# Performance work log

Hardware: AMD Instinct MI355X
Metric: run time of the kernel (lower is better)

Reference implementation:

```python
import jax, jax.numpy as jnp
import numpy as np

P = 1024   # number of partitions / local models (n_terms)
K = 9      # local neighborhood size (in_dim of each LocalDNN)
W = 10     # LocalDNN width
B = 16384  # batch
F = 1024   # input feature dim (lattice sites)


def setup_inputs() -> dict:
    key = jax.random.key(0)
    ks = jax.random.split(key, 9)
    x = jax.random.normal(ks[0], (B, F), dtype=jnp.float32)
    idx = jax.random.randint(ks[1], (P, K), 0, F)  # parameter_map: per-partition feature indices
    # stacked LocalDNN parameters (one tiny MLP per partition)
    s1 = 1.0 / np.sqrt(K)
    s2 = 1.0 / np.sqrt(W)
    W1 = jax.random.uniform(ks[2], (P, K, W), jnp.float32, -s1, s1)
    b1 = jax.random.uniform(ks[3], (P, W), jnp.float32, -s1, s1)
    W2 = jax.random.uniform(ks[4], (P, W, W), jnp.float32, -s2, s2)
    b2 = jax.random.uniform(ks[5], (P, W), jnp.float32, -s2, s2)
    W3 = jax.random.uniform(ks[6], (P, W), jnp.float32, -s2, s2)   # Linear(width,1) weight
    b3 = jax.random.uniform(ks[7], (P,), jnp.float32, -s2, s2)
    sP = 1.0 / np.sqrt(P)
    w_last = jax.random.uniform(ks[8], (P,), jnp.float32, -sP, sP)  # Linear(n_terms,1,bias=False)
    return {"x": x, "idx": idx, "W1": W1, "b1": b1, "W2": W2, "b2": b2,
            "W3": W3, "b3": b3, "w_last": w_last}


def reference(x, idx, W1, b1, W2, b2, W3, b3, w_last):
    # local_map: gather per-partition features -> [B, P, K]
    xg = x[:, idx]
    # LocalDNN (depth=2): Linear(K,W) -> tanh -> Linear(W,W) -> (dropout eval no-op) -> Linear(W,1)
    h = jnp.tanh(jnp.einsum('bpk,pkw->bpw', xg, W1) + b1)      # [B,P,W]
    h = jnp.einsum('bpw,pwv->bpv', h, W2) + b2                  # [B,P,W]
    local_out = jnp.einsum('bpw,pw->bp', h, W3) + b3            # concat of per-model outputs [B,P]
    y = local_out @ w_last                                      # last_layer, flatten -> [B]
    return jnp.stack((y, jnp.full_like(y, jnp.sum(jnp.abs(w_last)))))
```

## Files before the change

### kernel.cpp

```cpp
#include <hip/hip_runtime.h>
#include <cstdint>
#include <cstddef>

#define B_TOT   16384
#define F_DIM   1024
#define P_TOT   1024
#define K_IN    9
#define W_H     10
#define TB      128
#define THREADS 1024
#define NWAVE   16
#define PGRP    2
#define PPB     (P_TOT / PGRP)
#define LSTR    1028

#define REC_DW   64
#define TANH_C   2.8853900817779268f
#define F8_MAX   448.0f

typedef float f32x2 __attribute__((ext_vector_type(2)));

__device__ __forceinline__ float fast_exp2(float x) {
#if __has_builtin(__builtin_amdgcn_exp2f)
    return __builtin_amdgcn_exp2f(x);
#else
    return exp2f(x);
#endif
}
__device__ __forceinline__ float fast_rcp(float x) {
#if __has_builtin(__builtin_amdgcn_rcpf)
    return __builtin_amdgcn_rcpf(x);
#else
    return 1.0f / x;
#endif
}
__device__ __forceinline__ float sigm_r(float z) {
    return fast_rcp(fast_exp2(z) + 1.0f);
}
__device__ __forceinline__ f32x2 pkfma(f32x2 a, f32x2 b, f32x2 c) {
#if __has_builtin(__builtin_elementwise_fma)
    return __builtin_elementwise_fma(a, b, c);
#else
    return f32x2{fmaf(a[0], b[0], c[0]), fmaf(a[1], b[1], c[1])};
#endif
}
__device__ __forceinline__ f32x2 unpk8_w0(uint32_t u) {
#if __has_builtin(__builtin_amdgcn_cvt_pk_f32_fp8)
    auto v = __builtin_amdgcn_cvt_pk_f32_fp8((int)u, false);
    return f32x2{v[0], v[1]};
#else
    return f32x2{__builtin_amdgcn_cvt_f32_fp8((int)u, 0),
                 __builtin_amdgcn_cvt_f32_fp8((int)u, 1)};
#endif
}
__device__ __forceinline__ f32x2 unpk8_w1(uint32_t u) {
#if __has_builtin(__builtin_amdgcn_cvt_pk_f32_fp8)
    auto v = __builtin_amdgcn_cvt_pk_f32_fp8((int)u, true);
    return f32x2{v[0], v[1]};
#else
    return f32x2{__builtin_amdgcn_cvt_f32_fp8((int)u, 2),
                 __builtin_amdgcn_cvt_f32_fp8((int)u, 3)};
#endif
}
__device__ __forceinline__ f32x2 unpk8s(uint32_t u, int word) {
    return word ? unpk8_w1(u) : unpk8_w0(u);
}
__device__ __forceinline__ uint32_t pk2(float a0, float a1, float b0, float b1) {
    uint32_t u = (uint32_t)__builtin_amdgcn_cvt_pk_fp8_f32(a0, a1, 0, false);
    u = (uint32_t)__builtin_amdgcn_cvt_pk_fp8_f32(b0, b1, (int)u, true);
    return u;
}
__device__ __forceinline__ uint32_t comp4(const uint4& c, int j) {
    switch (j & 3) { case 0: return c.x; case 1: return c.y;
                     case 2: return c.z; default: return c.w; }
}
__device__ __forceinline__ uint32_t cvdw(const uint4* cv, int d) {
    return comp4(cv[d >> 2], d & 3);
}
__device__ __forceinline__ void ld_cv6(uint4* dst, const uint32_t* recp32) {
    const uint4* rv = reinterpret_cast<const uint4*>(recp32);
    asm("" : "+v"(rv));
    #pragma unroll
    for (int i = 0; i < 6; ++i) dst[i] = rv[i];
}

__device__ __forceinline__ uint32_t rec_dword(
    int p, int dw, const int* idx,
    const float* w1, const float* b1, const float* w2, const float* b2,
    const float* w3, const float* b3, const float* wl,
    float s1, float q1)
{
    if (dw < 9)  return (uint32_t)idx[p * 9 + dw];
    if (dw == 9) return __float_as_uint(s1 * TANH_C);
    if (dw < 20) return __float_as_uint(b1[p * 10 + (dw - 10)] * TANH_C);
    if (dw == 20) {
        float bb = b3[p];
        for (int v = 0; v < 10; ++v) bb = fmaf(b2[p * 10 + v], w3[v], bb);
        float s = 0.f;
        for (int w = 0; w < 10; ++w)
            for (int v = 0; v < 10; ++v)
                s = fmaf(w2[w * 10 + v], w3[v], s);
        return __float_as_uint(wl[p] * (s + bb));
    }
    if (dw < 31) {
        const int w = dw - 21;
        float s = 0.f;
        for (int v = 0; v < 10; ++v) s = fmaf(w2[w * 10 + v], w3[v], s);
        return __float_as_uint(-2.0f * wl[p] * s);
    }
    if (dw < 32) return 0;
    if (dw < 55) {
        const int d = dw - 32, t0 = 2 * d, t1 = t0 + 1;
        const int e0 = (t0 / 5) * 10 + 2 * (t0 % 5);
        const float a0 = w1[e0] * q1, a1 = w1[e0 + 1] * q1;
        float bq0 = 0.f, bq1 = 0.f;
        if (t1 < 45) {
            const int e1 = (t1 / 5) * 10 + 2 * (t1 % 5);
            bq0 = w1[e1] * q1; bq1 = w1[e1 + 1] * q1;
        }
        return pk2(a0, a1, bq0, bq1);
    }
    return 0;
}

__global__ __launch_bounds__(64)
void prep_quant(const int* __restrict__ idx,
                const float* __restrict__ W1, const float* __restrict__ b1,
                const float* __restrict__ W2, const float* __restrict__ b2,
                const float* __restrict__ W3, const float* __restrict__ b3,
                const float* __restrict__ wl, uint32_t* __restrict__ ws)
{
    const int p = blockIdx.x;
    const int l = threadIdx.x;
    const float* w1 = W1 + p * 90;
    const float* w2 = W2 + p * 100;
    const float* w3 = W3 + p * 10;

    float m1 = (l < 90) ? fabsf(w1[l]) : 0.0f;
    if (l + 64 < 90) m1 = fmaxf(m1, fabsf(w1[l + 64]));
    #pragma unroll
    for (int off = 32; off > 0; off >>= 1)
        m1 = fmaxf(m1, __shfl_xor(m1, off));
    m1 = fmaxf(m1, 1e-20f);
    const float s1 = m1 / F8_MAX, q1 = F8_MAX / m1;

    ws[(size_t)p * REC_DW + l] =
        rec_dword(p, l, idx, w1, b1, w2, b2, w3, b3, wl, s1, q1);
}

__device__ __forceinline__ void visit(
    const uint32_t* __restrict__ recs, const float* __restrict__ rfs,
    const uint4* cv,
    const unsigned char* __restrict__ row0, const unsigned char* __restrict__ row1,
    float& y0, float& y1)
{
    float xg0[K_IN], xg1[K_IN];
    #pragma unroll
    for (int k = 0; k < K_IN; ++k) {
        const int c = (int)recs[k];
        xg0[k] = __builtin_amdgcn_cvt_f32_fp8((int)row0[c], 0);
        xg1[k] = __builtin_amdgcn_cvt_f32_fp8((int)row1[c], 0);
    }

    f32x2 H0[5], H1[5];
    #pragma unroll
    for (int j = 0; j < 5; ++j) { H0[j] = f32x2{0.f, 0.f}; H1[j] = f32x2{0.f, 0.f}; }
    #pragma unroll
    for (int k = 0; k < K_IN; ++k) {
        const f32x2 xa = {xg0[k], xg0[k]};
        const f32x2 xb = {xg1[k], xg1[k]};
        #pragma unroll
        for (int j = 0; j < 5; ++j) {
            const int t = k * 5 + j;
            const f32x2 w = unpk8s(cvdw(cv, t >> 1), t & 1);
            H0[j] = pkfma(xa, w, H0[j]);
            H1[j] = pkfma(xb, w, H1[j]);
        }
    }
    const float s1c = rfs[9];
    const f32x2 s1p = {s1c, s1c};
    f32x2 r0[5], r1[5];
    #pragma unroll
    for (int j = 0; j < 5; ++j) {
        const f32x2 bj = {rfs[10 + 2 * j], rfs[11 + 2 * j]};
        const f32x2 z0 = pkfma(H0[j], s1p, bj);
        const f32x2 z1 = pkfma(H1[j], s1p, bj);
        r0[j] = f32x2{sigm_r(z0[0]), sigm_r(z0[1])};
        r1[j] = f32x2{sigm_r(z1[0]), sigm_r(z1[1])};
    }

    const float c0 = rfs[20];
    f32x2 A0 = {0.f, 0.f}, A1 = {0.f, 0.f};
    #pragma unroll
    for (int j = 0; j < 5; ++j) {
        const f32x2 cwj = {rfs[21 + 2 * j], rfs[22 + 2 * j]};
        A0 = pkfma(cwj, r0[j], A0);
        A1 = pkfma(cwj, r1[j], A1);
    }
    y0 += c0 + A0[0] + A0[1];
    y1 += c0 + A1[0] + A1[1];
}

__global__ __launch_bounds__(THREADS, 4)
void dnn_q8(const float* __restrict__ x, const uint32_t* __restrict__ ws,
            const float* __restrict__ wl, float* __restrict__ out)
{
    extern __shared__ unsigned char xs[];
    __shared__ float partial[NWAVE][TB];

    const int tid = threadIdx.x;
    const int b0  = blockIdx.x * TB;
    const int p0  = blockIdx.y * PPB;

    #pragma unroll
    for (int i = 0; i < (TB * (F_DIM / 4)) / THREADS; ++i) {
        const int q   = i * THREADS + tid;
        const int row = q >> 8;
        const int c4  = q & 255;
        const float4 v = *reinterpret_cast<const float4*>(
            x + (size_t)(b0 + row) * F_DIM + (c4 << 2));
        int pk = __builtin_amdgcn_cvt_pk_fp8_f32(v.x, v.y, 0, false);
        pk     = __builtin_amdgcn_cvt_pk_fp8_f32(v.z, v.w, pk, true);
        *reinterpret_cast<uint32_t*>(xs + row * LSTR + (c4 << 2)) = (uint32_t)pk;
    }
    __syncthreads();

    const int lane = tid & 63;
    const int wave = tid >> 6;
    const unsigned char* __restrict__ row0 = xs + lane * LSTR;
    const unsigned char* __restrict__ row1 = xs + (lane + 64) * LSTR;

    float y0 = 0.0f, y1 = 0.0f;

    uint4 cvA[6], cvB[6];
    ld_cv6(cvA, ws + (size_t)(p0 + wave) * REC_DW + 32);

    for (int jp = 0; jp < PPB / NWAVE; jp += 2) {
        const int pA = p0 + jp * NWAVE + wave;
        const int pB = pA + NWAVE;
        const int puA = __builtin_amdgcn_readfirstlane(pA);
        const int puB = __builtin_amdgcn_readfirstlane(pB);
        const uint32_t* __restrict__ recsA = ws + (size_t)puA * REC_DW;
        const uint32_t* __restrict__ recsB = ws + (size_t)puB * REC_DW;

        ld_cv6(cvB, ws + (size_t)pB * REC_DW + 32);
        visit(recsA, reinterpret_cast<const float*>(recsA), cvA, row0, row1, y0, y1);

        ld_cv6(cvA, ws + (size_t)(pB + NWAVE) * REC_DW + 32);
        visit(recsB, reinterpret_cast<const float*>(recsB), cvB, row0, row1, y0, y1);
    }

    partial[wave][lane]      = y0;
    partial[wave][lane + 64] = y1;
    __syncthreads();

    if (tid < TB) {
        float s = 0.0f;
        #pragma unroll
        for (int w = 0; w < NWAVE; ++w) s += partial[w][tid];
        atomicAdd(&out[b0 + tid], s);
    }

    if (blockIdx.y == 0 && tid < 64) {
        float sa = 0.0f;
        #pragma unroll
        for (int i = 0; i < P_TOT / 64; ++i) sa += fabsf(wl[tid + 64 * i]);
        #pragma unroll
        for (int off = 32; off > 0; off >>= 1) sa += __shfl_down(sa, off);
        sa = __shfl(sa, 0);
        out[B_TOT + b0 + tid]      = sa;
        out[B_TOT + b0 + 64 + tid] = sa;
    }
}

extern "C" void kernel_launch(void* const* d_in, const int* in_sizes, int n_in,
                              void* d_out, int out_size, void* d_ws, size_t ws_size,
                              hipStream_t stream)
{
    const float* x  = (const float*)d_in[0];
    const int*   idx= (const int*)  d_in[1];
    const float* W1 = (const float*)d_in[2];
    const float* b1 = (const float*)d_in[3];
    const float* W2 = (const float*)d_in[4];
    const float* b2 = (const float*)d_in[5];
    const float* W3 = (const float*)d_in[6];
    const float* b3 = (const float*)d_in[7];
    const float* wl = (const float*)d_in[8];
    float* out = (float*)d_out;
    uint32_t* ws = (uint32_t*)d_ws;

    (void)hipMemsetAsync(out, 0, B_TOT * sizeof(float), stream);

    prep_quant<<<P_TOT, 64, 0, stream>>>(idx, W1, b1, W2, b2, W3, b3, wl, ws);

    const int smem = TB * LSTR;
    (void)hipFuncSetAttribute(reinterpret_cast<const void*>(dnn_q8),
                              hipFuncAttributeMaxDynamicSharedMemorySize, smem);

    dim3 grid(B_TOT / TB, PGRP);
    dnn_q8<<<grid, THREADS, smem, stream>>>(x, ws, wl, out);
}
```

Measured before the change: 110.1 us.

## Stage per-partition records through LDS double buffer instead of scalar/register loads

Replaces per-partition record reads from global memory (scalar loads plus six uint4 vector registers holding the fp8 W1 weights) with a per-wave double-buffered LDS slot. Each lane loads one dword of the next record into LDS while the current one is computed. The aim is to cut register pressure and global load latency on the record fetches. In exchange, all weight and bias reads now go to LDS, which adds LDS traffic and latency alongside the gathers. The loop also has no explicit wave barrier between writing a slot and reading it, so it relies on wave-synchronous behaviour.

```diff
diff --git a/kernel.cpp b/kernel.cpp
--- a/kernel.cpp
+++ b/kernel.cpp
@@ -13,6 +13,7 @@
 #define PGRP    2
 #define PPB     (P_TOT / PGRP)
 #define LSTR    1028
+#define XS_BYTES (TB * LSTR)
 
 #define REC_DW   64
 #define TANH_C   2.8853900817779268f
@@ -69,19 +70,6 @@
     uint32_t u = (uint32_t)__builtin_amdgcn_cvt_pk_fp8_f32(a0, a1, 0, false);
     u = (uint32_t)__builtin_amdgcn_cvt_pk_fp8_f32(b0, b1, (int)u, true);
     return u;
-}
-__device__ __forceinline__ uint32_t comp4(const uint4& c, int j) {
-    switch (j & 3) { case 0: return c.x; case 1: return c.y;
-                     case 2: return c.z; default: return c.w; }
-}
-__device__ __forceinline__ uint32_t cvdw(const uint4* cv, int d) {
-    return comp4(cv[d >> 2], d & 3);
-}
-__device__ __forceinline__ void ld_cv6(uint4* dst, const uint32_t* recp32) {
-    const uint4* rv = reinterpret_cast<const uint4*>(recp32);
-    asm("" : "+v"(rv));
-    #pragma unroll
-    for (int i = 0; i < 6; ++i) dst[i] = rv[i];
 }
 
 __device__ __forceinline__ uint32_t rec_dword(
@@ -148,59 +136,6 @@
         rec_dword(p, l, idx, w1, b1, w2, b2, w3, b3, wl, s1, q1);
 }
 
-__device__ __forceinline__ void visit(
-    const uint32_t* __restrict__ recs, const float* __restrict__ rfs,
-    const uint4* cv,
-    const unsigned char* __restrict__ row0, const unsigned char* __restrict__ row1,
-    float& y0, float& y1)
-{
-    float xg0[K_IN], xg1[K_IN];
-    #pragma unroll
-    for (int k = 0; k < K_IN; ++k) {
-        const int c = (int)recs[k];
-        xg0[k] = __builtin_amdgcn_cvt_f32_fp8((int)row0[c], 0);
-        xg1[k] = __builtin_amdgcn_cvt_f32_fp8((int)row1[c], 0);
-    }
-
-    f32x2 H0[5], H1[5];
-    #pragma unroll
-    for (int j = 0; j < 5; ++j) { H0[j] = f32x2{0.f, 0.f}; H1[j] = f32x2{0.f, 0.f}; }
-    #pragma unroll
-    for (int k = 0; k < K_IN; ++k) {
-        const f32x2 xa = {xg0[k], xg0[k]};
-        const f32x2 xb = {xg1[k], xg1[k]};
-        #pragma unroll
-        for (int j = 0; j < 5; ++j) {
-            const int t = k * 5 + j;
-            const f32x2 w = unpk8s(cvdw(cv, t >> 1), t & 1);
-            H0[j] = pkfma(xa, w, H0[j]);
-            H1[j] = pkfma(xb, w, H1[j]);
-        }
-    }
-    const float s1c = rfs[9];
-    const f32x2 s1p = {s1c, s1c};
-    f32x2 r0[5], r1[5];
-    #pragma unroll
-    for (int j = 0; j < 5; ++j) {
-        const f32x2 bj = {rfs[10 + 2 * j], rfs[11 + 2 * j]};
-        const f32x2 z0 = pkfma(H0[j], s1p, bj);
-        const f32x2 z1 = pkfma(H1[j], s1p, bj);
-        r0[j] = f32x2{sigm_r(z0[0]), sigm_r(z0[1])};
-        r1[j] = f32x2{sigm_r(z1[0]), sigm_r(z1[1])};
-    }
-
-    const float c0 = rfs[20];
-    f32x2 A0 = {0.f, 0.f}, A1 = {0.f, 0.f};
-    #pragma unroll
-    for (int j = 0; j < 5; ++j) {
-        const f32x2 cwj = {rfs[21 + 2 * j], rfs[22 + 2 * j]};
-        A0 = pkfma(cwj, r0[j], A0);
-        A1 = pkfma(cwj, r1[j], A1);
-    }
-    y0 += c0 + A0[0] + A0[1];
-    y1 += c0 + A1[0] + A1[1];
-}
-
 __global__ __launch_bounds__(THREADS, 4)
 void dnn_q8(const float* __restrict__ x, const uint32_t* __restrict__ ws,
             const float* __restrict__ wl, float* __restrict__ out)
@@ -229,25 +164,71 @@
     const int wave = tid >> 6;
     const unsigned char* __restrict__ row0 = xs + lane * LSTR;
     const unsigned char* __restrict__ row1 = xs + (lane + 64) * LSTR;
+    uint32_t* slots = reinterpret_cast<uint32_t*>(xs + XS_BYTES) + wave * (2 * REC_DW);
 
     float y0 = 0.0f, y1 = 0.0f;
 
-    uint4 cvA[6], cvB[6];
-    ld_cv6(cvA, ws + (size_t)(p0 + wave) * REC_DW + 32);
-
-    for (int jp = 0; jp < PPB / NWAVE; jp += 2) {
-        const int pA = p0 + jp * NWAVE + wave;
-        const int pB = pA + NWAVE;
-        const int puA = __builtin_amdgcn_readfirstlane(pA);
-        const int puB = __builtin_amdgcn_readfirstlane(pB);
-        const uint32_t* __restrict__ recsA = ws + (size_t)puA * REC_DW;
-        const uint32_t* __restrict__ recsB = ws + (size_t)puB * REC_DW;
-
-        ld_cv6(cvB, ws + (size_t)pB * REC_DW + 32);
-        visit(recsA, reinterpret_cast<const float*>(recsA), cvA, row0, row1, y0, y1);
-
-        ld_cv6(cvA, ws + (size_t)(pB + NWAVE) * REC_DW + 32);
-        visit(recsB, reinterpret_cast<const float*>(recsB), cvB, row0, row1, y0, y1);
+    {
+        const uint32_t v = ws[(size_t)(p0 + wave) * REC_DW + lane];
+        slots[lane] = v;
+    }
+    int cur = 0;
+
+    for (int jp = 0; jp < PPB / NWAVE; ++jp) {
+        const int p = p0 + jp * NWAVE + wave;
+        const uint32_t* __restrict__ rec = slots + cur * REC_DW;
+        const float*    __restrict__ rf  = reinterpret_cast<const float*>(rec);
+
+        const uint32_t stg = ws[(size_t)(p + NWAVE) * REC_DW + lane];
+
+        float xg0[K_IN], xg1[K_IN];
+        #pragma unroll
+        for (int k = 0; k < K_IN; ++k) {
+            const int c = (int)rec[k];
+            xg0[k] = __builtin_amdgcn_cvt_f32_fp8((int)row0[c], 0);
+            xg1[k] = __builtin_amdgcn_cvt_f32_fp8((int)row1[c], 0);
+        }
+
+        f32x2 H0[5], H1[5];
+        #pragma unroll
+        for (int j = 0; j < 5; ++j) { H0[j] = f32x2{0.f, 0.f}; H1[j] = f32x2{0.f, 0.f}; }
+        #pragma unroll
+        for (int k = 0; k < K_IN; ++k) {
+            const f32x2 xa = {xg0[k], xg0[k]};
+            const f32x2 xb = {xg1[k], xg1[k]};
+            #pragma unroll
+            for (int j = 0; j < 5; ++j) {
+                const int t = k * 5 + j;
+                const f32x2 w = unpk8s(rec[32 + (t >> 1)], t & 1);
+                H0[j] = pkfma(xa, w, H0[j]);
+                H1[j] = pkfma(xb, w, H1[j]);
+            }
+        }
+        const float s1c = rf[9];
+        const f32x2 s1p = {s1c, s1c};
+        f32x2 r0[5], r1[5];
+        #pragma unroll
+        for (int j = 0; j < 5; ++j) {
+            const f32x2 bj = {rf[10 + 2 * j], rf[11 + 2 * j]};
+            const f32x2 z0 = pkfma(H0[j], s1p, bj);
+            const f32x2 z1 = pkfma(H1[j], s1p, bj);
+            r0[j] = f32x2{sigm_r(z0[0]), sigm_r(z0[1])};
+            r1[j] = f32x2{sigm_r(z1[0]), sigm_r(z1[1])};
+        }
+
+        const float c0 = rf[20];
+        f32x2 A0 = {0.f, 0.f}, A1 = {0.f, 0.f};
+        #pragma unroll
+        for (int j = 0; j < 5; ++j) {
+            const f32x2 cwj = {rf[21 + 2 * j], rf[22 + 2 * j]};
+            A0 = pkfma(cwj, r0[j], A0);
+            A1 = pkfma(cwj, r1[j], A1);
+        }
+        y0 += c0 + A0[0] + A0[1];
+        y1 += c0 + A1[0] + A1[1];
+
+        slots[(cur ^ 1) * REC_DW + lane] = stg;
+        cur ^= 1;
     }
 
     partial[wave][lane]      = y0;
@@ -293,7 +274,7 @@
 
     prep_quant<<<P_TOT, 64, 0, stream>>>(idx, W1, b1, W2, b2, W3, b3, wl, ws);
 
-    const int smem = TB * LSTR;
+    const int smem = XS_BYTES + NWAVE * 2 * REC_DW * 4;
     (void)hipFuncSetAttribute(reinterpret_cast<const void*>(dnn_q8),
                               hipFuncAttributeMaxDynamicSharedMemorySize, smem);
 
```

After: 105.0 us. 4.6% less time.
